# Performance work log

Measured on AMD Instinct MI355X. Metric: run time of the kernel, lower is better.

The kernel has to match this reference:

```python
import jax, jax.numpy as jnp
import numpy as np
from jax import lax

FPLANE = 64
T = 8          # num_segments
HEADS = 4
EPS = 1e-5


def _conv2d(x, w, b):
    # x: [N,C,H,W], w: [O,I,kh,kw]
    y = lax.conv_general_dilated(x, w, (1, 1), 'SAME',
                                 dimension_numbers=('NCHW', 'OIHW', 'NCHW'))
    return y + b[None, :, None, None]


def _conv3d_grouped(x, w, b, groups):
    # x: [N,C,D,H,W], w: [O, C//groups, kd,kh,kw]
    y = lax.conv_general_dilated(x, w, (1, 1, 1), 'SAME',
                                 dimension_numbers=('NCDHW', 'OIDHW', 'NCDHW'),
                                 feature_group_count=groups)
    return y + b[None, :, None, None, None]


def setup_inputs() -> dict:
    key = jax.random.key(0)
    ks = jax.random.split(key, 5)
    N, C, H, W = T * 16, FPLANE, 56, 56
    x = jax.random.normal(ks[0], (N, C, H, W), dtype=jnp.float32)
    attn_w = jax.random.normal(ks[1], (HEADS, C, 3, 3), dtype=jnp.float32) * 0.05
    attn_b = jax.random.normal(ks[2], (HEADS,), dtype=jnp.float32) * 0.05
    bn_gamma = jnp.ones((C,), dtype=jnp.float32)
    bn_beta = jnp.zeros((C,), dtype=jnp.float32)
    conv3d_w = jax.random.normal(ks[3], (2, C // 2, 3, 3, 3), dtype=jnp.float32) * 0.05
    conv3d_b = jax.random.normal(ks[4], (2,), dtype=jnp.float32) * 0.05
    return {'x': x, 'attn_w': attn_w, 'attn_b': attn_b,
            'bn_gamma': bn_gamma, 'bn_beta': bn_beta,
            'conv3d_w': conv3d_w, 'conv3d_b': conv3d_b}


def reference(x, attn_w, attn_b, bn_gamma, bn_beta, conv3d_w, conv3d_b):
    N, C, H, W = x.shape
    B = N // T
    half = C // 2
    quarter = C // 4

    # spatial attention: conv2d -> ReLU -> Sigmoid, per-head gating
    attn = jax.nn.sigmoid(jax.nn.relu(_conv2d(x, attn_w, attn_b)))  # [N,HEADS,H,W]
    xh = x.reshape(N, HEADS, C // HEADS, H, W) * attn[:, :, None]
    x2 = xh.reshape(N, C, H, W)

    # [B*T,C,H,W] -> [B,C,T,H,W]
    x5 = x2.reshape(B, T, C, H, W).transpose(0, 2, 1, 3, 4)

    # BatchNorm3d (training-mode batch statistics) + ReLU
    mean = jnp.mean(x5, axis=(0, 2, 3, 4), keepdims=True)
    var = jnp.var(x5, axis=(0, 2, 3, 4), keepdims=True)
    x_bn = (x5 - mean) * lax.rsqrt(var + EPS)
    x_bn = x_bn * bn_gamma[None, :, None, None, None] + bn_beta[None, :, None, None, None]
    x_bn_relu = jax.nn.relu(x_bn)

    # grouped conv3d gate (2 groups, 1 output channel each), tanh
    gate = jnp.tanh(_conv3d_grouped(x_bn_relu, conv3d_w, conv3d_b, groups=2))  # [B,2,T,H,W]
    g1 = gate[:, 0:1]
    g2 = gate[:, 1:2]

    x_g1 = x5[:, :half]
    x_g2 = x5[:, half:]
    y1 = g1 * x_g1
    y2 = g2 * x_g2
    r1 = x_g1 - y1
    r2 = x_g2 - y2

    pad_t = ((0, 0), (0, 0), (0, 1), (0, 0), (0, 0))
    pad_b = ((0, 0), (0, 0), (1, 0), (0, 0), (0, 0))
    y1 = jnp.pad(y1[:, :, 1:], pad_t) + r1   # left shift in time, zero pad
    y2 = jnp.pad(y2[:, :, :-1], pad_b) + r2  # right shift in time, zero pad

    # interleave sub-halves: view [B,2,C/4,T,H,W] -> permute -> [B,C/2,T,H,W]
    def interleave(y):
        return (y.reshape(B, 2, quarter, T, H, W)
                 .transpose(0, 2, 1, 3, 4, 5)
                 .reshape(B, half, T, H, W))

    y = jnp.concatenate([interleave(y1), interleave(y2)], axis=1)  # [B,C,T,H,W]
    return y.transpose(0, 2, 1, 3, 4).reshape(N, C, H, W)
```

## Files before the change

### kernel.cpp

```cpp
#include <hip/hip_runtime.h>
#include <hip/hip_bf16.h>

#define HW 3136
#define CTOT 64
#define NTOT 128
#define BB 16
#define TTT 8

static __device__ __forceinline__ float bf2f(unsigned short u) {
    union { unsigned int ui; float f; } v;
    v.ui = ((unsigned int)u) << 16;
    return v.f;
}
static __device__ __forceinline__ unsigned short f2bf(float f) {
    union { float f; unsigned int u; } v;
    v.f = f;
    unsigned int u = v.u;
    unsigned int r = (u + 0x7fffu + ((u >> 16) & 1u)) >> 16;
    return (unsigned short)r;
}

__global__ __launch_bounds__(128) void k_attn(const float* __restrict__ x,
                                              const float* __restrict__ aw,
                                              const float* __restrict__ ab,
                                              float* __restrict__ attn,
                                              float* __restrict__ stats) {
    const int tile = blockIdx.x % 49;
    const int n = blockIdx.x / 49;
    const int chunk = threadIdx.x >> 4;
    const int qi = threadIdx.x & 15;
    const int quad = tile * 16 + qi;
    const int q = quad % 14;
    const int h = quad / 14;
    const int w0 = q * 4;

    __shared__ float wl[2304];
    __shared__ float l[8][16][17];
    __shared__ float4 abuf[4][16];

    const float* xn = x + (size_t)n * CTOT * HW;
    const int c0 = chunk * 8;

    auto loadrows = [&](int c, float r[3][6]) {
#pragma unroll
        for (int dh = 0; dh < 3; ++dh) {
            const int hh = h + dh - 1;
            const bool v = (hh >= 0) && (hh < 56);
            const float* row = xn + c * HW + (v ? hh : h) * 56 + w0;
            const float m = v ? 1.f : 0.f;
            const float4 mid = *(const float4*)row;
            const float e0 = row[(q > 0) ? -1 : 0] * ((q > 0) ? m : 0.f);
            const float e5 = row[(q < 13) ? 4 : 3] * ((q < 13) ? m : 0.f);
            r[dh][0] = e0;
            r[dh][1] = mid.x * m; r[dh][2] = mid.y * m;
            r[dh][3] = mid.z * m; r[dh][4] = mid.w * m;
            r[dh][5] = e5;
        }
    };

    float bufA[3][6], bufB[3][6];
    loadrows(c0, bufA);

#pragma unroll
    for (int i = 0; i < 18; ++i) {
        const int idx = threadIdx.x + i * 128;
        const int hd = idx & 3;
        const int kw = (idx >> 2) % 3;
        const int dh = (idx / 12) % 3;
        const int c = idx / 36;
        wl[idx] = aw[hd * 576 + c * 9 + dh * 3 + kw];
    }
    __syncthreads();

    float acc[4][4];
#pragma unroll
    for (int hd = 0; hd < 4; ++hd)
#pragma unroll
        for (int j = 0; j < 4; ++j) acc[hd][j] = 0.f;

    float midst[8][4];

#pragma unroll
    for (int i = 0; i < 8; ++i) {
        float (*cur)[6] = (i & 1) ? bufB : bufA;
        float (*nxt)[6] = (i & 1) ? bufA : bufB;
        if (i < 7) loadrows(c0 + i + 1, nxt);

        midst[i][0] = cur[1][1]; midst[i][1] = cur[1][2];
        midst[i][2] = cur[1][3]; midst[i][3] = cur[1][4];

        const int c = c0 + i;
#pragma unroll
        for (int dh = 0; dh < 3; ++dh) {
            const float* wb = &wl[c * 36 + dh * 12];
            const float4 wk0 = *(const float4*)(wb);
            const float4 wk1 = *(const float4*)(wb + 4);
            const float4 wk2 = *(const float4*)(wb + 8);
#pragma unroll
            for (int j = 0; j < 4; ++j) {
                const float a0 = cur[dh][j], a1 = cur[dh][j + 1], a2 = cur[dh][j + 2];
                acc[0][j] = fmaf(a0, wk0.x, fmaf(a1, wk1.x, fmaf(a2, wk2.x, acc[0][j])));
                acc[1][j] = fmaf(a0, wk0.y, fmaf(a1, wk1.y, fmaf(a2, wk2.y, acc[1][j])));
                acc[2][j] = fmaf(a0, wk0.z, fmaf(a1, wk1.z, fmaf(a2, wk2.z, acc[2][j])));
                acc[3][j] = fmaf(a0, wk0.w, fmaf(a1, wk1.w, fmaf(a2, wk2.w, acc[3][j])));
            }
        }
    }

    float* mine = &l[chunk][qi][0];
#pragma unroll
    for (int hd = 0; hd < 4; ++hd)
#pragma unroll
        for (int j = 0; j < 4; ++j) mine[hd * 4 + j] = acc[hd][j];
    __syncthreads();

    if (threadIdx.x < 64) {
        const int hd = threadIdx.x >> 4;
        const int rq = threadIdx.x & 15;
        float s0 = ab[hd], s1 = s0, s2 = s0, s3 = s0;
#pragma unroll
        for (int cch = 0; cch < 8; ++cch) {
            const float* p = &l[cch][rq][hd * 4];
            s0 += p[0]; s1 += p[1]; s2 += p[2]; s3 += p[3];
        }
        float4 o;
        o.x = s0 > 0.f ? 1.f / (1.f + __expf(-s0)) : 0.5f;
        o.y = s1 > 0.f ? 1.f / (1.f + __expf(-s1)) : 0.5f;
        o.z = s2 > 0.f ? 1.f / (1.f + __expf(-s2)) : 0.5f;
        o.w = s3 > 0.f ? 1.f / (1.f + __expf(-s3)) : 0.5f;
        *(float4*)(attn + (size_t)(n * 4 + hd) * HW + (tile * 16 + rq) * 4) = o;
        abuf[hd][rq] = o;
    }
    __syncthreads();

    const int head = chunk >> 1;
    const float4 a4 = abuf[head][qi];
    float s[8], sq[8];
#pragma unroll
    for (int i = 0; i < 8; ++i) {
        const float v0 = midst[i][0] * a4.x;
        const float v1 = midst[i][1] * a4.y;
        const float v2 = midst[i][2] * a4.z;
        const float v3 = midst[i][3] * a4.w;
        s[i] = v0 + v1 + v2 + v3;
        sq[i] = v0 * v0 + v1 * v1 + v2 * v2 + v3 * v3;
    }
#pragma unroll
    for (int i = 0; i < 8; ++i) { mine[i] = s[i]; mine[8 + i] = sq[i]; }
    __syncthreads();
    {
        const int ch2 = threadIdx.x >> 4;
        const int k = threadIdx.x & 15;
        float t = 0.f;
#pragma unroll
        for (int qq = 0; qq < 16; ++qq) t += l[ch2][qq][k];
        const int cc = ch2 * 8 + (k & 7);
        const int rep = blockIdx.x & 15;
        atomicAdd(&stats[rep * 128 + (k >> 3) * 64 + cc], t);
    }
}

__global__ void k_finalize(const float* __restrict__ stats,
                           const float* __restrict__ gamma,
                           const float* __restrict__ beta,
                           float* __restrict__ ss) {
    const int c = threadIdx.x;
    float S = 0.f, Q = 0.f;
#pragma unroll
    for (int r = 0; r < 16; ++r) {
        S += stats[r * 128 + c];
        Q += stats[r * 128 + 64 + c];
    }
    const float cnt = 401408.0f;
    const float mean = S / cnt;
    const float var = Q / cnt - mean * mean;
    const float scale = gamma[c] * rsqrtf(var + 1e-5f);
    ss[c] = scale;
    ss[64 + c] = beta[c] - mean * scale;
}

__global__ __launch_bounds__(256) void k_xbnr(const float* __restrict__ x,
                                              const float* __restrict__ attn,
                                              const float* __restrict__ ss,
                                              unsigned short* __restrict__ xbnr) {
    const int s = blockIdx.x & 7;
    const int n = blockIdx.x >> 3;
    const int base_sp = s * 392;

    __shared__ float al[4 * 392];
    __shared__ float ssl[128];
    for (int i = threadIdx.x; i < 392; i += 256) {
        const int hd = i / 98;
        const int j = i - hd * 98;
        ((float4*)al)[hd * 98 + j] =
            *(const float4*)(attn + (size_t)(n * 4 + hd) * HW + base_sp + j * 4);
    }
    if (threadIdx.x < 128) ssl[threadIdx.x] = ss[threadIdx.x];
    __syncthreads();

    for (int wi = threadIdx.x; wi < 6272; wi += 256) {
        const int c = wi / 98;
        const int j = wi - c * 98;
        const float sc = ssl[c], sh = ssl[64 + c];
        const float4 xv = *(const float4*)(x + (size_t)(n * 64 + c) * HW + base_sp + j * 4);
        const float4 av = ((const float4*)al)[(c >> 4) * 98 + j];
        ushort4 o;
        o.x = f2bf(fmaxf(fmaf(xv.x * av.x, sc, sh), 0.f));
        o.y = f2bf(fmaxf(fmaf(xv.y * av.y, sc, sh), 0.f));
        o.z = f2bf(fmaxf(fmaf(xv.z * av.z, sc, sh), 0.f));
        o.w = f2bf(fmaxf(fmaf(xv.w * av.w, sc, sh), 0.f));
        *(ushort4*)(xbnr + (size_t)(n * 64 + c) * HW + base_sp + j * 4) = o;
    }
}

__global__ __launch_bounds__(128) void k_conv3d(const unsigned short* __restrict__ xbnr,
                                                const float* __restrict__ w3,
                                                const float* __restrict__ b3,
                                                float* __restrict__ gate) {
    const int tile = blockIdx.x % 49;
    const int oc = (blockIdx.x / 49) & 1;
    const int b = blockIdx.x / 98;
    const int chunk = threadIdx.x >> 4;
    const int qi = threadIdx.x & 15;
    const int quad = tile * 16 + qi;
    const int q = quad % 14;
    const int h = quad / 14;
    const int w0 = q * 4;

    __shared__ float wlds[864];
    for (int i = threadIdx.x; i < 864; i += 128) wlds[i] = w3[oc * 864 + i];
    __syncthreads();

    float acc[8][4];
#pragma unroll
    for (int t = 0; t < 8; ++t)
#pragma unroll
        for (int j = 0; j < 4; ++j) acc[t][j] = 0.f;

    const int ic0 = chunk * 4;
    for (int ic = ic0; ic < ic0 + 4; ++ic) {
        const int c = oc * 32 + ic;
        const unsigned short* cbase = xbnr + (size_t)(b * 8 * 64 + c) * HW;
        const float* wic = &wlds[ic * 27];
#pragma unroll
        for (int tt = 0; tt < 8; ++tt) {
            const unsigned short* plane = cbase + (size_t)tt * (64 * HW);
#pragma unroll
            for (int dh = 0; dh < 3; ++dh) {
                const int hh = h + dh - 1;
                if (hh < 0 || hh >= 56) continue;
                const unsigned short* row = plane + hh * 56 + w0;
                const ushort4 mid = *(const ushort4*)row;
                const float f0 = (q > 0) ? bf2f(row[-1]) : 0.f;
                const float f1 = bf2f(mid.x), f2 = bf2f(mid.y);
                const float f3 = bf2f(mid.z), f4 = bf2f(mid.w);
                const float f5 = (q < 13) ? bf2f(row[4]) : 0.f;
#pragma unroll
                for (int dt = 0; dt < 3; ++dt) {
                    const int t = tt + 1 - dt;
                    if (t < 0 || t > 7) continue;
                    const float* wp = wic + dt * 9 + dh * 3;
                    const float wa = wp[0], wb = wp[1], wc = wp[2];
                    acc[t][0] = fmaf(f0, wa, fmaf(f1, wb, fmaf(f2, wc, acc[t][0])));
                    acc[t][1] = fmaf(f1, wa, fmaf(f2, wb, fmaf(f3, wc, acc[t][1])));
                    acc[t][2] = fmaf(f2, wa, fmaf(f3, wb, fmaf(f4, wc, acc[t][2])));
                    acc[t][3] = fmaf(f3, wa, fmaf(f4, wb, fmaf(f5, wc, acc[t][3])));
                }
            }
        }
    }

    __shared__ float4 l4[8 * 16 * 9];
    float4* mine = &l4[(chunk * 16 + qi) * 9];
#pragma unroll
    for (int t = 0; t < 8; ++t) {
        float4 v;
        v.x = acc[t][0]; v.y = acc[t][1]; v.z = acc[t][2]; v.w = acc[t][3];
        mine[t] = v;
    }
    __syncthreads();

    const int rt = threadIdx.x >> 4;
    const int rq = threadIdx.x & 15;
    float4 s = l4[(0 * 16 + rq) * 9 + rt];
#pragma unroll
    for (int c = 1; c < 8; ++c) {
        const float4 v = l4[(c * 16 + rq) * 9 + rt];
        s.x += v.x; s.y += v.y; s.z += v.z; s.w += v.w;
    }
    const float bb = b3[oc];
    float4 o;
    o.x = tanhf(s.x + bb);
    o.y = tanhf(s.y + bb);
    o.z = tanhf(s.z + bb);
    o.w = tanhf(s.w + bb);
    const int outquad = tile * 16 + rq;
    *(float4*)(gate + (size_t)((b * 2 + oc) * 8 + rt) * HW + outquad * 4) = o;
}

__global__ __launch_bounds__(256) void k_final(const float* __restrict__ x,
                                               const float* __restrict__ attn,
                                               const float* __restrict__ gate,
                                               float* __restrict__ out) {
    const int gt = blockIdx.x * 256 + threadIdx.x;
    const int q = gt % 14;
    int r = gt / 14;
    const int h = r % 56;
    r /= 56;
    const int co = r & 63;
    const int b = r >> 6;
    const int sp = h * 56 + q * 4;

    int cs, grp;
    if (co < 32) {
        cs = ((co & 1) << 4) | (co >> 1);
        grp = 0;
    } else {
        const int cc = co - 32;
        cs = 32 + (((cc & 1) << 4) | (cc >> 1));
        grp = 1;
    }
    const int head = cs >> 4;

    float4 x2[8], g[8];
#pragma unroll
    for (int t = 0; t < 8; ++t) {
        const int n = b * 8 + t;
        const float4 xv = *(const float4*)(x + (size_t)(n * 64 + cs) * HW + sp);
        const float4 av = *(const float4*)(attn + (size_t)(n * 4 + head) * HW + sp);
        const float4 gv = *(const float4*)(gate + (size_t)((b * 2 + grp) * 8 + t) * HW + sp);
        x2[t].x = xv.x * av.x;
        x2[t].y = xv.y * av.y;
        x2[t].z = xv.z * av.z;
        x2[t].w = xv.w * av.w;
        g[t] = gv;
    }
#pragma unroll
    for (int t = 0; t < 8; ++t) {
        float4 o;
        o.x = x2[t].x * (1.f - g[t].x);
        o.y = x2[t].y * (1.f - g[t].y);
        o.z = x2[t].z * (1.f - g[t].z);
        o.w = x2[t].w * (1.f - g[t].w);
        if (grp == 0) {
            if (t < 7) {
                o.x += x2[t + 1].x * g[t + 1].x;
                o.y += x2[t + 1].y * g[t + 1].y;
                o.z += x2[t + 1].z * g[t + 1].z;
                o.w += x2[t + 1].w * g[t + 1].w;
            }
        } else {
            if (t > 0) {
                o.x += x2[t - 1].x * g[t - 1].x;
                o.y += x2[t - 1].y * g[t - 1].y;
                o.z += x2[t - 1].z * g[t - 1].z;
                o.w += x2[t - 1].w * g[t - 1].w;
            }
        }
        *(float4*)(out + (size_t)((b * 8 + t) * 64 + co) * HW + sp) = o;
    }
}

extern "C" void kernel_launch(void* const* d_in, const int* in_sizes, int n_in,
                              void* d_out, int out_size, void* d_ws, size_t ws_size,
                              hipStream_t stream) {
    const float* x = (const float*)d_in[0];
    const float* aw = (const float*)d_in[1];
    const float* ab = (const float*)d_in[2];
    const float* gamma = (const float*)d_in[3];
    const float* beta = (const float*)d_in[4];
    const float* w3 = (const float*)d_in[5];
    const float* b3 = (const float*)d_in[6];
    float* out = (float*)d_out;

    char* ws = (char*)d_ws;
    unsigned short* xbnr = (unsigned short*)ws;
    float* attn = (float*)(ws + 51380224);
    float* gate = (float*)(ws + 57802752);
    float* stats = (float*)(ws + 57802752);
    float* ss = (float*)(ws + 61014528);

    hipMemsetAsync(stats, 0, 8192, stream);
    k_attn<<<6272, 128, 0, stream>>>(x, aw, ab, attn, stats);
    k_finalize<<<1, 64, 0, stream>>>(stats, gamma, beta, ss);
    k_xbnr<<<1024, 256, 0, stream>>>(x, attn, ss, xbnr);
    k_conv3d<<<1568, 128, 0, stream>>>(xbnr, w3, b3, gate);
    k_final<<<3136, 256, 0, stream>>>(x, attn, gate, out);
}
```

Before: 358.6 us.

## Merge memset and finalize into neighbouring kernels, prepack attn weights, remap k_final

Replaces the memset plus k_finalize launches with a small repack kernel that zeroes the stats buffer and pre-permutes the attention conv weights, and folds the BN finalize math into each k_xbnr block. k_attn now loads the weights with a plain contiguous copy instead of computing scattered indices. k_final is remapped so that each block handles one (batch, row, channel half), with 448 threads. The aim is fewer launches and cheaper per-block setup, at the cost of every k_xbnr block redoing the 64-channel stats reduction.

```diff
diff --git a/kernel.cpp b/kernel.cpp
--- a/kernel.cpp
+++ b/kernel.cpp
@@ -20,8 +20,20 @@
     return (unsigned short)r;
 }
 
+__global__ void k_repack(const float* __restrict__ aw, float* __restrict__ wpk,
+                         float* __restrict__ stats) {
+    const int idx = blockIdx.x * 256 + threadIdx.x;
+    if (idx < 2048) stats[idx] = 0.f;
+    if (idx >= 2304) return;
+    const int hd = idx & 3;
+    const int kw = (idx >> 2) % 3;
+    const int dh = (idx / 12) % 3;
+    const int c = idx / 36;
+    wpk[idx] = aw[hd * 576 + c * 9 + dh * 3 + kw];
+}
+
 __global__ __launch_bounds__(128) void k_attn(const float* __restrict__ x,
-                                              const float* __restrict__ aw,
+                                              const float* __restrict__ wpk,
                                               const float* __restrict__ ab,
                                               float* __restrict__ attn,
                                               float* __restrict__ stats) {
@@ -62,14 +74,7 @@
     loadrows(c0, bufA);
 
 #pragma unroll
-    for (int i = 0; i < 18; ++i) {
-        const int idx = threadIdx.x + i * 128;
-        const int hd = idx & 3;
-        const int kw = (idx >> 2) % 3;
-        const int dh = (idx / 12) % 3;
-        const int c = idx / 36;
-        wl[idx] = aw[hd * 576 + c * 9 + dh * 3 + kw];
-    }
+    for (int i = 0; i < 18; ++i) wl[threadIdx.x + i * 128] = wpk[threadIdx.x + i * 128];
     __syncthreads();
 
     float acc[4][4];
@@ -160,28 +165,11 @@
     }
 }
 
-__global__ void k_finalize(const float* __restrict__ stats,
-                           const float* __restrict__ gamma,
-                           const float* __restrict__ beta,
-                           float* __restrict__ ss) {
-    const int c = threadIdx.x;
-    float S = 0.f, Q = 0.f;
-#pragma unroll
-    for (int r = 0; r < 16; ++r) {
-        S += stats[r * 128 + c];
-        Q += stats[r * 128 + 64 + c];
-    }
-    const float cnt = 401408.0f;
-    const float mean = S / cnt;
-    const float var = Q / cnt - mean * mean;
-    const float scale = gamma[c] * rsqrtf(var + 1e-5f);
-    ss[c] = scale;
-    ss[64 + c] = beta[c] - mean * scale;
-}
-
 __global__ __launch_bounds__(256) void k_xbnr(const float* __restrict__ x,
                                               const float* __restrict__ attn,
-                                              const float* __restrict__ ss,
+                                              const float* __restrict__ stats,
+                                              const float* __restrict__ gamma,
+                                              const float* __restrict__ beta,
                                               unsigned short* __restrict__ xbnr) {
     const int s = blockIdx.x & 7;
     const int n = blockIdx.x >> 3;
@@ -195,7 +183,21 @@
         ((float4*)al)[hd * 98 + j] =
             *(const float4*)(attn + (size_t)(n * 4 + hd) * HW + base_sp + j * 4);
     }
-    if (threadIdx.x < 128) ssl[threadIdx.x] = ss[threadIdx.x];
+    if (threadIdx.x < 64) {
+        const int c = threadIdx.x;
+        float S = 0.f, Q = 0.f;
+#pragma unroll
+        for (int r = 0; r < 16; ++r) {
+            S += stats[r * 128 + c];
+            Q += stats[r * 128 + 64 + c];
+        }
+        const float cnt = 401408.0f;
+        const float mean = S / cnt;
+        const float var = Q / cnt - mean * mean;
+        const float scale = gamma[c] * rsqrtf(var + 1e-5f);
+        ssl[c] = scale;
+        ssl[64 + c] = beta[c] - mean * scale;
+    }
     __syncthreads();
 
     for (int wi = threadIdx.x; wi < 6272; wi += 256) {
@@ -298,63 +300,61 @@
     *(float4*)(gate + (size_t)((b * 2 + oc) * 8 + rt) * HW + outquad * 4) = o;
 }
 
-__global__ __launch_bounds__(256) void k_final(const float* __restrict__ x,
+__global__ __launch_bounds__(448) void k_final(const float* __restrict__ x,
                                                const float* __restrict__ attn,
                                                const float* __restrict__ gate,
                                                float* __restrict__ out) {
-    const int gt = blockIdx.x * 256 + threadIdx.x;
-    const int q = gt % 14;
-    int r = gt / 14;
-    const int h = r % 56;
-    r /= 56;
-    const int co = r & 63;
-    const int b = r >> 6;
+    const int hg = blockIdx.x & 1;
+    const int h = (blockIdx.x >> 1) % 56;
+    const int b = blockIdx.x / 112;
+    const int q = threadIdx.x % 14;
+    const int col = threadIdx.x / 14;
+    const int co = hg * 32 + col;
     const int sp = h * 56 + q * 4;
 
-    int cs, grp;
+    int cs;
     if (co < 32) {
         cs = ((co & 1) << 4) | (co >> 1);
-        grp = 0;
     } else {
         const int cc = co - 32;
         cs = 32 + (((cc & 1) << 4) | (cc >> 1));
-        grp = 1;
-    }
+    }
+    const int grp = hg;
     const int head = cs >> 4;
 
-    float4 x2[8], g[8];
+    float4 x2v[8], g[8];
 #pragma unroll
     for (int t = 0; t < 8; ++t) {
         const int n = b * 8 + t;
         const float4 xv = *(const float4*)(x + (size_t)(n * 64 + cs) * HW + sp);
         const float4 av = *(const float4*)(attn + (size_t)(n * 4 + head) * HW + sp);
         const float4 gv = *(const float4*)(gate + (size_t)((b * 2 + grp) * 8 + t) * HW + sp);
-        x2[t].x = xv.x * av.x;
-        x2[t].y = xv.y * av.y;
-        x2[t].z = xv.z * av.z;
-        x2[t].w = xv.w * av.w;
+        x2v[t].x = xv.x * av.x;
+        x2v[t].y = xv.y * av.y;
+        x2v[t].z = xv.z * av.z;
+        x2v[t].w = xv.w * av.w;
         g[t] = gv;
     }
 #pragma unroll
     for (int t = 0; t < 8; ++t) {
         float4 o;
-        o.x = x2[t].x * (1.f - g[t].x);
-        o.y = x2[t].y * (1.f - g[t].y);
-        o.z = x2[t].z * (1.f - g[t].z);
-        o.w = x2[t].w * (1.f - g[t].w);
+        o.x = x2v[t].x * (1.f - g[t].x);
+        o.y = x2v[t].y * (1.f - g[t].y);
+        o.z = x2v[t].z * (1.f - g[t].z);
+        o.w = x2v[t].w * (1.f - g[t].w);
         if (grp == 0) {
             if (t < 7) {
-                o.x += x2[t + 1].x * g[t + 1].x;
-                o.y += x2[t + 1].y * g[t + 1].y;
-                o.z += x2[t + 1].z * g[t + 1].z;
-                o.w += x2[t + 1].w * g[t + 1].w;
+                o.x += x2v[t + 1].x * g[t + 1].x;
+                o.y += x2v[t + 1].y * g[t + 1].y;
+                o.z += x2v[t + 1].z * g[t + 1].z;
+                o.w += x2v[t + 1].w * g[t + 1].w;
             }
         } else {
             if (t > 0) {
-                o.x += x2[t - 1].x * g[t - 1].x;
-                o.y += x2[t - 1].y * g[t - 1].y;
-                o.z += x2[t - 1].z * g[t - 1].z;
-                o.w += x2[t - 1].w * g[t - 1].w;
+                o.x += x2v[t - 1].x * g[t - 1].x;
+                o.y += x2v[t - 1].y * g[t - 1].y;
+                o.z += x2v[t - 1].z * g[t - 1].z;
+                o.w += x2v[t - 1].w * g[t - 1].w;
             }
         }
         *(float4*)(out + (size_t)((b * 8 + t) * 64 + co) * HW + sp) = o;
@@ -378,12 +378,11 @@
     float* attn = (float*)(ws + 51380224);
     float* gate = (float*)(ws + 57802752);
     float* stats = (float*)(ws + 57802752);
-    float* ss = (float*)(ws + 61014528);
-
-    hipMemsetAsync(stats, 0, 8192, stream);
-    k_attn<<<6272, 128, 0, stream>>>(x, aw, ab, attn, stats);
-    k_finalize<<<1, 64, 0, stream>>>(stats, gamma, beta, ss);
-    k_xbnr<<<1024, 256, 0, stream>>>(x, attn, ss, xbnr);
+    float* wpk = (float*)(ws + 61015040);
+
+    k_repack<<<9, 256, 0, stream>>>(aw, wpk, stats);
+    k_attn<<<6272, 128, 0, stream>>>(x, wpk, ab, attn, stats);
+    k_xbnr<<<1024, 256, 0, stream>>>(x, attn, stats, gamma, beta, xbnr);
     k_conv3d<<<1568, 128, 0, stream>>>(xbnr, w3, b3, gate);
-    k_final<<<3136, 256, 0, stream>>>(x, attn, gate, out);
-}
+    k_final<<<1792, 448, 0, stream>>>(x, attn, gate, out);
+}
```

After: 370.6 us. +3.3%, slower.
